# Performance work log

Hardware: AMD Instinct MI355X
Metric: run time of the kernel (lower is better)

Reference implementation:

```python
import jax, jax.numpy as jnp
import numpy as np

N, E, B, D, H, L = 50000, 800000, 16, 64, 128, 2


def _lin(h, w, b):
    return h @ w + b


def _scatter_mean(v, idx, n):
    s = jax.ops.segment_sum(v, idx, num_segments=n)
    c = jax.ops.segment_sum(jnp.ones((v.shape[0],), v.dtype), idx, num_segments=n)
    return s / jnp.maximum(c, 1.0)[:, None]


def setup_inputs() -> dict:
    key = jax.random.key(0)
    ks = iter(jax.random.split(key, 40))

    def p(*shape):
        return jax.random.normal(next(ks), shape, dtype=jnp.float32) * 0.05

    inp = {
        "x": jax.random.normal(next(ks), (N, D), dtype=jnp.float32),
        "edge_attr": jax.random.normal(next(ks), (E, D), dtype=jnp.float32),
        "u": jax.random.normal(next(ks), (B, D), dtype=jnp.float32),
        "e_w1": p(L, 4 * D, H), "e_b1": p(L, H),
        "e_w2": p(L, H, H), "e_b2": p(L, H),
        "e_w3": p(L, H, D), "e_b3": p(L, D),
        "n1_w1": p(L, 2 * D, H), "n1_b1": p(L, H),
        "n1_w2": p(L, H, H), "n1_b2": p(L, H),
        "n2_w1": p(L, D + H + D, H), "n2_b1": p(L, H),
        "n2_w2": p(L, H, D), "n2_b2": p(L, D),
        "g_w1": p(L, 3 * D, H), "g_b1": p(L, H),
        "g_w2": p(L, H, D), "g_b2": p(L, D),
        "edge_index": jax.random.randint(next(ks), (2, E), 0, N, dtype=jnp.int32),
        "batch": jnp.sort(jax.random.randint(next(ks), (N,), 0, B, dtype=jnp.int32)),
    }
    return inp


def _forward(x, edge_attr, u, params, edge_index, batch):
    row, col = edge_index[0], edge_index[1]
    eb = batch[row]  # [E] graph id per edge
    x0, e0, u0 = x, edge_attr, u
    for l in range(L):
        (e_w1, e_b1, e_w2, e_b2, e_w3, e_b3,
         n1_w1, n1_b1, n1_w2, n1_b2,
         n2_w1, n2_b1, n2_w2, n2_b2,
         g_w1, g_b1, g_w2, g_b2) = [pm[l] for pm in params]
        # Edge model: [E, e+2n+u] -> MLP -> [E, D]
        h = jnp.concatenate([x[row], x[col], edge_attr, u[eb]], axis=1)
        h = jax.nn.relu(_lin(h, e_w1, e_b1))
        h = jax.nn.relu(_lin(h, e_w2, e_b2))
        edge_attr = _lin(h, e_w3, e_b3)
        # Node model: gather src node + edge, MLP1, scatter_mean onto dest, MLP2
        se = jnp.concatenate([x[row], edge_attr], axis=1)  # [E, 2D]
        se = _lin(jax.nn.relu(_lin(se, n1_w1, n1_b1)), n1_w2, n1_b2)
        agg = _scatter_mean(se, col, N)  # [N, H]
        xh = jnp.concatenate([x, agg, u[batch]], axis=1)
        x = _lin(jax.nn.relu(_lin(xh, n2_w1, n2_b1)), n2_w2, n2_b2)
        # Global model: per-graph means of updated nodes/edges
        e_agg = _scatter_mean(edge_attr, eb, B)
        n_agg = _scatter_mean(x, batch, B)
        uh = jnp.concatenate([u, n_agg, e_agg], axis=1)
        u = _lin(jax.nn.relu(_lin(uh, g_w1, g_b1)), g_w2, g_b2)
    return x + x0, edge_attr + e0, u + u0


def reference(x, edge_attr, u, e_w1, e_b1, e_w2, e_b2, e_w3, e_b3, n1_w1, n1_b1, n1_w2, n1_b2, n2_w1, n2_b1, n2_w2, n2_b2, g_w1, g_b1, g_w2, g_b2, edge_index, batch):
    params = (e_w1, e_b1, e_w2, e_b2, e_w3, e_b3,
              n1_w1, n1_b1, n1_w2, n1_b2,
              n2_w1, n2_b1, n2_w2, n2_b2,
              g_w1, g_b1, g_w2, g_b2)
    return _forward(x, edge_attr, u, params, edge_index, batch)
```

## Files before the change

kernel.cpp:

```cpp
#include <hip/hip_runtime.h>

#define N_NODES 50000
#define E_EDGES 800000
#define NG 16
#define DD 64
#define HH 128
#define NB_SCAN 49
#define EREP 32

typedef __attribute__((ext_vector_type(8))) __bf16 bf16x8;
typedef __attribute__((ext_vector_type(4))) float f32x4;
typedef unsigned int uint;
typedef unsigned short ushort;
typedef __attribute__((ext_vector_type(4))) uint uint4v;

#define MFMA16(a,b,c) __builtin_amdgcn_mfma_f32_16x16x32_bf16((a),(b),(c),0,0,0)

__device__ __forceinline__ ushort f2bf(float f){
  uint u = __builtin_bit_cast(uint, f);
  u += 0x7fffu + ((u >> 16) & 1u);
  return (ushort)(u >> 16);
}
__device__ __forceinline__ uint pk2(float a, float b){
  return (uint)f2bf(a) | ((uint)f2bf(b) << 16);
}
__device__ __forceinline__ float bflo(uint u){ return __builtin_bit_cast(float, u << 16); }
__device__ __forceinline__ float bfhi(uint u){ return __builtin_bit_cast(float, u & 0xffff0000u); }

__device__ __forceinline__ void bar(){
  asm volatile("s_waitcnt lgkmcnt(0)" ::: "memory");
  __builtin_amdgcn_s_barrier();
}

__device__ __forceinline__ bf16x8 ldfrag(const char* base, int row, int byteoff){
  uint4v v = *(const uint4v*)(base + row*256 + (byteoff ^ ((row & 7) << 4)));
  return __builtin_bit_cast(bf16x8, v);
}
__device__ __forceinline__ uint4v ld_chunk(const char* base, int row, int c16){
  return *(const uint4v*)(base + row*256 + ((c16*16) ^ ((row & 7) << 4)));
}
__device__ __forceinline__ void st_h(char* base, int row, int col, float v){
  *(ushort*)(base + row*256 + ((col*2) ^ ((row & 7) << 4))) = f2bf(v);
}
__device__ __forceinline__ void st_chunk(char* base, int row, int c16, uint4v v){
  *(uint4v*)(base + row*256 + ((c16*16) ^ ((row & 7) << 4))) = v;
}
__device__ __forceinline__ bf16x8 ldfrag128(const char* base, int row, int byteoff){
  uint4v v = *(const uint4v*)(base + row*128 + (byteoff ^ ((row & 7) << 4)));
  return __builtin_bit_cast(bf16x8, v);
}
__device__ __forceinline__ uint4v ld_chunk128(const char* base, int row, int c16){
  return *(const uint4v*)(base + row*128 + ((c16*16) ^ ((row & 7) << 4)));
}
__device__ __forceinline__ void st_chunk128(char* base, int row, int c16, uint4v v){
  *(uint4v*)(base + row*128 + ((c16*16) ^ ((row & 7) << 4))) = v;
}
__device__ __forceinline__ void st_h128(char* base, int row, int col, float v){
  *(ushort*)(base + row*128 + ((col*2) ^ ((row & 7) << 4))) = f2bf(v);
}
__device__ __forceinline__ void pack16_128(char* dst, int r, int c16, const float* src){
  float4 lo = *(const float4*)src;
  float4 hi = *(const float4*)(src + 4);
  uint4v v; v.x = pk2(lo.x, lo.y); v.y = pk2(lo.z, lo.w);
  v.z = pk2(hi.x, hi.y); v.w = pk2(hi.z, hi.w);
  st_chunk128(dst, r, c16, v);
}

__device__ __forceinline__ void stage_b(char* sB, const ushort* wt,
                                        int Nout, int Ktot, int koff, int t, int stride){
  for (int task = t; task < Nout*16; task += stride){
    int n = task >> 4, c = task & 15;
    uint4v v = *(const uint4v*)(wt + (long)n*Ktot + koff + c*8);
    st_chunk(sB, n, c, v);
  }
}
template<int NT>
__device__ __forceinline__ void gemm_acc(const char* A, const char* B,
                                         int wv, int l15, int lhi, f32x4* acc){
  #pragma unroll
  for (int kt = 0; kt < 4; ++kt){
    bf16x8 a = ldfrag(A, wv*16 + l15, kt*64 + lhi*16);
    #pragma unroll
    for (int n = 0; n < NT; ++n){
      bf16x8 bb = ldfrag(B, n*16 + l15, kt*64 + lhi*16);
      acc[n] = MFMA16(a, bb, acc[n]);
    }
  }
}
template<int NT, bool RELU>
__device__ __forceinline__ void epi_lds(char* dst, const f32x4* acc, const float* bias,
                                        int wv, int l15, int lhi){
  #pragma unroll
  for (int n = 0; n < NT; ++n){
    float bv = bias[n*16 + l15];
    #pragma unroll
    for (int j = 0; j < 4; ++j){
      int r = wv*16 + lhi*4 + j;
      float v = acc[n][j] + bv;
      if (RELU) v = fmaxf(v, 0.f);
      st_h(dst, r, n*16 + l15, v);
    }
  }
}

__global__ void convert_x(const float* __restrict__ x, ushort* __restrict__ xbf){
  int i = blockIdx.x*256 + threadIdx.x;
  if (i < (N_NODES*DD)/8){
    float4 lo = *(const float4*)(x + (long)i*8);
    float4 hi = *(const float4*)(x + (long)i*8 + 4);
    uint4v v; v.x = pk2(lo.x, lo.y); v.y = pk2(lo.z, lo.w);
    v.z = pk2(hi.x, hi.y); v.w = pk2(hi.z, hi.w);
    *(uint4v*)(xbf + (long)i*8) = v;
  }
}

__global__ void pack_weights(const float* __restrict__ e1, const float* __restrict__ e2,
                             const float* __restrict__ e3, const float* __restrict__ n12,
                             const float* __restrict__ n21, const float* __restrict__ n22,
                             ushort* __restrict__ out){
  int idx = blockIdx.x * 256 + threadIdx.x;
  int l = idx / 114688, r = idx % 114688;
  const float* src; int K, N, off;
  if      (r <  32768){ src = e1;  K = 256; N = 128; off = 0; }
  else if (r <  49152){ src = e2;  K = 128; N = 128; off = 32768; }
  else if (r <  57344){ src = e3;  K = 128; N = 64;  off = 49152; }
  else if (r <  73728){ src = n12; K = 128; N = 128; off = 57344; }
  else if (r < 106496){ src = n21; K = 256; N = 128; off = 73728; }
  else                { src = n22; K = 128; N = 64;  off = 106496; }
  int q = r - off; int k = q / N; int n = q % N;
  out[(long)l*139264 + off + n*K + k] = f2bf(src[(long)l*K*N + q]);
}

__global__ void make_wc(const float* __restrict__ n1w1, const float* __restrict__ ew3,
                        const float* __restrict__ n1b1, const float* __restrict__ eb3,
                        ushort* __restrict__ packed, float* __restrict__ biasc){
  int l = blockIdx.x, t = threadIdx.x;
  const float* W1 = n1w1 + (long)l*128*128;
  const float* W3 = ew3 + (long)l*128*64;
  ushort* wc = packed + (long)l*139264 + 114688;
  for (int i = t; i < 8192; i += 256){
    int k = i >> 7, n = i & 127;
    wc[n*192 + k] = f2bf(W1[k*128 + n]);
  }
  for (int i = t; i < 16384; i += 256){
    int k2 = i >> 7, n = i & 127;
    float s = 0.f;
    for (int m = 0; m < 64; ++m) s += W3[k2*64 + m] * W1[(64 + m)*128 + n];
    wc[n*192 + 64 + k2] = f2bf(s);
  }
  if (t < 128){
    float s = n1b1[l*128 + t];
    for (int m = 0; m < 64; ++m) s += eb3[l*64 + m] * W1[(64 + m)*128 + t];
    biasc[l*128 + t] = s;
  }
}

__global__ void hist_kernel(const int* __restrict__ edge_index, const int* __restrict__ batch,
                            int* __restrict__ deg, float* __restrict__ cnt_eb){
  __shared__ float h[NG];
  int t = threadIdx.x;
  if (t < NG) h[t] = 0.f;
  __syncthreads();
  int e = blockIdx.x * 256 + t;
  if (e < E_EDGES){
    atomicAdd(deg + edge_index[E_EDGES + e], 1);
    atomicAdd(&h[batch[edge_index[e]]], 1.f);
  }
  __syncthreads();
  if (t < NG) atomicAdd(cnt_eb + t, h[t]);
}
__global__ void count_nodes_kernel(const int* __restrict__ batch, float* __restrict__ cnt_b){
  __shared__ float h[NG];
  int t = threadIdx.x;
  if (t < NG) h[t] = 0.f;
  __syncthreads();
  int n = blockIdx.x * 256 + t;
  if (n < N_NODES) atomicAdd(&h[batch[n]], 1.f);
  __syncthreads();
  if (t < NG) atomicAdd(cnt_b + t, h[t]);
}
__global__ void scan_a(const int* __restrict__ deg, int* __restrict__ bsum){
  __shared__ int red[1024];
  int i = blockIdx.x*1024 + threadIdx.x;
  red[threadIdx.x] = (i < N_NODES) ? deg[i] : 0;
  __syncthreads();
  for (int s = 512; s > 0; s >>= 1){
    if ((int)threadIdx.x < s) red[threadIdx.x] += red[threadIdx.x + s];
    __syncthreads();
  }
  if (threadIdx.x == 0) bsum[blockIdx.x] = red[0];
}
__global__ void scan_b(const int* __restrict__ bsum, int* __restrict__ bbase){
  if (threadIdx.x == 0){
    int run = 0;
    for (int b = 0; b < NB_SCAN; ++b){ int v = bsum[b]; bbase[b] = run; run += v; }
  }
}
__global__ void scan_c(const int* __restrict__ deg, const int* __restrict__ bbase,
                       int* __restrict__ off, int* __restrict__ cursor){
  __shared__ int sc[1024];
  int i = blockIdx.x*1024 + threadIdx.x;
  int v = (i < N_NODES) ? deg[i] : 0;
  sc[threadIdx.x] = v;
  __syncthreads();
  for (int d = 1; d < 1024; d <<= 1){
    int add = ((int)threadIdx.x >= d) ? sc[threadIdx.x - d] : 0;
    __syncthreads();
    sc[threadIdx.x] += add;
    __syncthreads();
  }
  if (i < N_NODES){
    int ex = sc[threadIdx.x] - v + bbase[blockIdx.x];
    off[i] = ex; cursor[i] = ex;
  }
}
__global__ void fill_kernel(const int* __restrict__ edge_index, int* __restrict__ cursor,
                            int* __restrict__ pos){
  int e = blockIdx.x*256 + threadIdx.x;
  if (e < E_EDGES){
    int c = edge_index[E_EDGES + e];
    pos[e] = atomicAdd(&cursor[c], 1);
  }
}

template<bool CSR, bool EBF>
__global__ __launch_bounds__(256, 2) void edge_fused(
    const ushort* __restrict__ xbf, const float* e_f32, const ushort* e_bf,
    const float* __restrict__ u_cur,
    const int* __restrict__ ei, const int* __restrict__ batch,
    const int* __restrict__ pos_arr,
    const ushort* __restrict__ w1t, const ushort* __restrict__ w2t,
    const ushort* __restrict__ w3t, const ushort* __restrict__ wct,
    const ushort* __restrict__ w5t,
    const float* __restrict__ be1, const float* __restrict__ be2,
    const float* __restrict__ be3, const float* __restrict__ biasc,
    const float* __restrict__ bn12,
    float* e_outf, const float* __restrict__ e_resid,
    ushort* __restrict__ se_buf, float* __restrict__ agg_sum,
    float* __restrict__ e_agg_rep, int has_resid)
{
  __shared__ __align__(16) char lds[73728];
  __shared__ float sEagg[NG*DD];
  __shared__ int sRow[64];
  __shared__ int sCol[64];
  __shared__ int sDst[64];
  char* X  = lds;
  char* A0 = lds + 8192;
  char* A1 = lds + 16384;
  char* W0 = lds + 24576;
  char* W1 = lds + 40960;
  char* OV = lds + 57344;
  const int t = threadIdx.x;
  const int wv = t >> 6, l15 = t & 15, lhi = (t >> 4) & 3;
  const int ebase = blockIdx.x * 64;

  auto WSTAGE = [&](char* W, const ushort* wt, int K, int coff){
    #pragma unroll
    for (int it = 0; it < 4; ++it){
      int task = t + it*256, n = task >> 3, c16 = task & 7;
      st_chunk128(W, n, c16, *(const uint4v*)(wt + (long)n*K + coff + c16*8));
    }
  };

  if (t < 64){
    int r = ei[ebase + t];
    int c = ei[E_EDGES + ebase + t];
    sRow[t] = r | (batch[r] << 16);
    sCol[t] = c;
    sDst[t] = CSR ? pos_arr[ebase + t] : c;
  }
  WSTAGE(W0, w1t, 256, 0);
  WSTAGE(W1, w1t, 256, 64);
  bf16x8 b3[4][4];
  #pragma unroll
  for (int n = 0; n < 4; ++n)
    #pragma unroll
    for (int kk = 0; kk < 4; ++kk)
      b3[n][kk] = *(const bf16x8*)(w3t + (long)(n*16 + l15)*128 + kk*32 + lhi*8);
  for (int i = t; i < NG*DD; i += 256) sEagg[i] = 0.f;
  __syncthreads();

  uint4v xr[2], xc[2], eu[2];
  float4 ef[4];
  #pragma unroll
  for (int it = 0; it < 2; ++it){
    int task = t + it*256, r = task >> 3, c16 = task & 7;
    xr[it] = *(const uint4v*)(xbf + (long)(sRow[r] & 0xffff)*DD + c16*8);
    xc[it] = *(const uint4v*)(xbf + (long)sCol[r]*DD + c16*8);
    if (EBF) eu[it] = *(const uint4v*)(e_bf + (long)(ebase + r)*HH + c16*8);
    else { ef[2*it]   = *(const float4*)(e_f32 + (long)(ebase + r)*DD + c16*8);
           ef[2*it+1] = *(const float4*)(e_f32 + (long)(ebase + r)*DD + c16*8 + 4); }
  }
  #pragma unroll
  for (int it = 0; it < 2; ++it){
    int task = t + it*256, r = task >> 3, c16 = task & 7;
    st_chunk128(X, r, c16, xr[it]);
  }
  __syncthreads();

  f32x4 acc1[8];
  #pragma unroll
  for (int n = 0; n < 8; ++n) acc1[n] = f32x4{0,0,0,0};
  auto MM128 = [&](const char* A, const char* W, f32x4* acc){
    #pragma unroll
    for (int kt = 0; kt < 2; ++kt){
      bf16x8 a = ldfrag128(A, wv*16 + l15, kt*64 + lhi*16);
      #pragma unroll
      for (int n = 0; n < 8; ++n){
        bf16x8 bb = ldfrag128(W, n*16 + l15, kt*64 + lhi*16);
        acc[n] = MFMA16(a, bb, acc[n]);
      }
    }
  };
  f32x4 acc3[4];
  #pragma unroll
  for (int n = 0; n < 4; ++n) acc3[n] = f32x4{0,0,0,0};
  auto MMOV = [&](int cbase, const char* W, f32x4* acc){
    #pragma unroll
    for (int kt = 0; kt < 2; ++kt){
      bf16x8 a = ldfrag(OV, wv*16 + l15, cbase + kt*64 + lhi*16);
      #pragma unroll
      for (int n = 0; n < 8; ++n){
        bf16x8 bb = ldfrag128(W, n*16 + l15, kt*64 + lhi*16);
        acc[n] = MFMA16(a, bb, acc[n]);
      }
    }
  };
  auto MMOV3 = [&](int cbase, const char* W, f32x4* acc, int kkb){
    #pragma unroll
    for (int kt = 0; kt < 2; ++kt){
      bf16x8 a = ldfrag(OV, wv*16 + l15, cbase + kt*64 + lhi*16);
      #pragma unroll
      for (int n = 0; n < 8; ++n){
        bf16x8 bb = ldfrag128(W, n*16 + l15, kt*64 + lhi*16);
        acc[n] = MFMA16(a, bb, acc[n]);
      }
      #pragma unroll
      for (int n = 0; n < 4; ++n)
        acc3[n] = MFMA16(a, b3[n][kkb + kt], acc3[n]);
    }
  };
  auto EPI = [&](const float* bias, const f32x4* acc, bool relu){
    #pragma unroll
    for (int n = 0; n < 8; ++n){
      int col = n*16 + l15;
      float bv = bias[col];
      #pragma unroll
      for (int j = 0; j < 4; ++j){
        float v = acc[n][j] + bv;
        if (relu) v = fmaxf(v, 0.f);
        st_h(OV, wv*16 + lhi*4 + j, col, v);
      }
    }
  };

  MM128(X, W0, acc1);
  #pragma unroll
  for (int it = 0; it < 2; ++it){
    int task = t + it*256, r = task >> 3, c16 = task & 7;
    st_chunk128(A0, r, c16, xc[it]);
  }
  bar();
  MM128(A0, W1, acc1);
  WSTAGE(W0, w1t, 256, 128);
  #pragma unroll
  for (int it = 0; it < 2; ++it){
    int task = t + it*256, r = task >> 3, c16 = task & 7;
    if (EBF) st_chunk128(A1, r, c16, eu[it]);
    else {
      uint4v v; v.x = pk2(ef[2*it].x, ef[2*it].y);     v.y = pk2(ef[2*it].z, ef[2*it].w);
      v.z = pk2(ef[2*it+1].x, ef[2*it+1].y); v.w = pk2(ef[2*it+1].z, ef[2*it+1].w);
      st_chunk128(A1, r, c16, v);
    }
  }
  bar();
  MM128(A1, W0, acc1);
  WSTAGE(W1, w1t, 256, 192);
  #pragma unroll
  for (int it = 0; it < 2; ++it){
    int task = t + it*256, r = task >> 3, c16 = task & 7;
    pack16_128(A0, r, c16, u_cur + (long)(sRow[r] >> 16)*DD + c16*8);
  }
  bar();
  MM128(A0, W1, acc1);
  WSTAGE(W0, w2t, 128, 0);
  EPI(be1, acc1, true);
  bar();
  f32x4 acc2[8];
  #pragma unroll
  for (int n = 0; n < 8; ++n) acc2[n] = f32x4{0,0,0,0};
  MMOV(0, W0, acc2);
  WSTAGE(W1, w2t, 128, 64);
  bar();
  MMOV(128, W1, acc2);
  WSTAGE(W0, wct, 192, 0);
  EPI(be2, acc2, true);
  bar();
  f32x4 acc4[8];
  #pragma unroll
  for (int n = 0; n < 8; ++n) acc4[n] = f32x4{0,0,0,0};
  MM128(X, W0, acc4);
  WSTAGE(W1, wct, 192, 64);
  bar();
  MMOV3(0, W1, acc4, 0);
  WSTAGE(W0, wct, 192, 128);
  bar();
  MMOV3(128, W0, acc4, 2);
  WSTAGE(W1, w5t, 128, 0);
  EPI(biasc, acc4, true);
  bar();
  f32x4 acc5[8];
  #pragma unroll
  for (int n = 0; n < 8; ++n) acc5[n] = f32x4{0,0,0,0};
  MMOV(0, W1, acc5);
  WSTAGE(W0, w5t, 128, 64);
  bar();
  MMOV(128, W0, acc5);
  bar();

  if (CSR){
    #pragma unroll
    for (int n = 0; n < 8; ++n){
      int col = n*16 + l15;
      float bv = bn12[col];
      #pragma unroll
      for (int j = 0; j < 4; ++j)
        st_h(OV, wv*16 + lhi*4 + j, col, acc5[n][j] + bv);
    }
    if (!has_resid){
      #pragma unroll
      for (int n = 0; n < 4; ++n){
        int col = n*16 + l15;
        float bv = be3[col];
        #pragma unroll
        for (int j = 0; j < 4; ++j){
          int row = wv*16 + lhi*4 + j;
          float v = acc3[n][j] + bv;
          st_h128(A0, row, col, v);
          atomicAdd(&sEagg[(sRow[row] >> 16)*DD + col], v);
        }
      }
    } else {
      #pragma unroll
      for (int n = 0; n < 4; ++n){
        int col = n*16 + l15;
        float bv = be3[col];
        #pragma unroll
        for (int j = 0; j < 4; ++j){
          int row = wv*16 + lhi*4 + j;
          float v = acc3[n][j] + bv;
          long eg = (long)(ebase + row)*DD + col;
          e_outf[eg] = v + e_resid[eg];
          atomicAdd(&sEagg[(sRow[row] >> 16)*DD + col], v);
        }
      }
    }
    bar();
    #pragma unroll
    for (int it = 0; it < 4; ++it){
      int task = t + it*256, r = task >> 4, c16 = task & 15;
      *(uint4v*)(se_buf + (long)sDst[r]*HH + c16*8) = ld_chunk(OV, r, c16);
    }
    if (!has_resid){
      ushort* ebf_out = (ushort*)e_outf;
      #pragma unroll
      for (int it = 0; it < 2; ++it){
        int task = t + it*256, r = task >> 3, c16 = task & 7;
        *(uint4v*)(ebf_out + (long)(ebase + r)*HH + c16*8) = ld_chunk128(A0, r, c16);
      }
    }
  } else {
    #pragma unroll
    for (int n = 0; n < 8; ++n){
      int col = n*16 + l15;
      float bv = bn12[col];
      #pragma unroll
      for (int j = 0; j < 4; ++j){
        int row = wv*16 + lhi*4 + j;
        atomicAdd(agg_sum + (long)sDst[row]*HH + col, acc5[n][j] + bv);
      }
    }
    #pragma unroll
    for (int n = 0; n < 4; ++n){
      int col = n*16 + l15;
      float bv = be3[col];
      #pragma unroll
      for (int j = 0; j < 4; ++j){
        int row = wv*16 + lhi*4 + j;
        float v = acc3[n][j] + bv;
        long eg = (long)(ebase + row)*DD + col;
        e_outf[eg] = has_resid ? (v + e_resid[eg]) : v;
        atomicAdd(&sEagg[(sRow[row] >> 16)*DD + col], v);
      }
    }
  }
  __syncthreads();
  float* dst = e_agg_rep + (long)(blockIdx.x & (EREP - 1))*NG*DD;
  for (int i = t; i < NG*DD; i += 256) atomicAdd(dst + i, sEagg[i]);
}

template<bool CSR>
__global__ __launch_bounds__(256, 2) void node_kernel(
    const float* __restrict__ x_cur, const float* __restrict__ u_cur,
    const float* __restrict__ x_resid, const int* __restrict__ batch,
    const ushort* __restrict__ se_buf, const int* __restrict__ deg,
    const int* __restrict__ off, const float* __restrict__ agg_sum,
    const ushort* __restrict__ w_n21, const ushort* __restrict__ w_n22,
    const float* __restrict__ b_n21, const float* __restrict__ b_n22,
    float* __restrict__ x_out, ushort* __restrict__ xbf_out,
    float* __restrict__ n_agg, int has_resid)
{
  __shared__ __align__(16) char sA[16384];
  __shared__ __align__(16) char sB[32768];
  __shared__ __align__(16) char sH[16384];
  __shared__ int sBat[64], sDeg[64], sOff[64];
  __shared__ float sRinv[64];
  __shared__ float sNagg[NG*DD];

  const int t = threadIdx.x;
  const int wv = t >> 6, ln = t & 63, l15 = ln & 15, lhi = ln >> 4;
  const int n0 = blockIdx.x * 64;

  if (t < 64){
    int nd = n0 + t;
    int ok = nd < N_NODES;
    sBat[t] = ok ? batch[nd] : 0;
    int d = ok ? deg[nd] : 0;
    sDeg[t] = d;
    sOff[t] = ok ? off[nd] : 0;
    sRinv[t] = 1.f / fmaxf((float)d, 1.f);
  }
  for (int i = t; i < NG*DD; i += 256) sNagg[i] = 0.f;
  __syncthreads();

  float s[32];
  const int r4 = t >> 2, q = t & 3;
  if (CSR){
    #pragma unroll
    for (int k = 0; k < 32; ++k) s[k] = 0.f;
    int d = sDeg[r4], o = sOff[r4];
    for (int i = 0; i < d; ++i){
      const ushort* src = se_buf + (long)(o + i)*HH + q*32;
      #pragma unroll
      for (int c = 0; c < 4; ++c){
        uint4v v = *(const uint4v*)(src + c*8);
        #pragma unroll
        for (int jj = 0; jj < 4; ++jj){
          s[c*8 + jj*2]     += bflo(v[jj]);
          s[c*8 + jj*2 + 1] += bfhi(v[jj]);
        }
      }
    }
    float riv = sRinv[r4];
    #pragma unroll
    for (int k = 0; k < 32; ++k) s[k] *= riv;
  }

  f32x4 acc[8];
  #pragma unroll
  for (int n = 0; n < 8; ++n) acc[n] = f32x4{0.f,0.f,0.f,0.f};

  for (int half = 0; half < 2; ++half){
    if (CSR){
      for (int task = t; task < 512; task += 256){
        int r = task >> 3, c = task & 7;
        int nd = n0 + r;
        bool ok = nd < N_NODES;
        float4 lo = {0,0,0,0}, hi = {0,0,0,0};
        if (ok){
          const float* src = (half == 0) ? (x_cur + (long)nd*DD + c*8)
                                         : (u_cur + (long)sBat[r]*DD + c*8);
          lo = *(const float4*)src; hi = *(const float4*)(src + 4);
        }
        uint4v v; v.x = pk2(lo.x, lo.y); v.y = pk2(lo.z, lo.w);
        v.z = pk2(hi.x, hi.y); v.w = pk2(hi.z, hi.w);
        st_chunk(sA, r, (half == 0) ? c : (8 + c), v);
      }
      if ((half == 0 && q < 2) || (half == 1 && q >= 2)){
        int cbase = (half == 0) ? (8 + q*4) : ((q - 2)*4);
        #pragma unroll
        for (int cc = 0; cc < 4; ++cc){
          uint4v v;
          v.x = pk2(s[cc*8+0], s[cc*8+1]); v.y = pk2(s[cc*8+2], s[cc*8+3]);
          v.z = pk2(s[cc*8+4], s[cc*8+5]); v.w = pk2(s[cc*8+6], s[cc*8+7]);
          st_chunk(sA, r4, cbase + cc, v);
        }
      }
    } else {
      for (int task = t; task < 1024; task += 256){
        int r = task >> 4, c = task & 15;
        int nd = n0 + r;
        bool ok = nd < N_NODES;
        float scale = 1.f;
        const float* src;
        if (half == 0){
          if (c < 8) src = x_cur + (long)nd*DD + c*8;
          else { src = agg_sum + (long)nd*HH + (c-8)*8; scale = sRinv[r]; }
        } else {
          if (c < 8){ src = agg_sum + (long)nd*HH + 64 + c*8; scale = sRinv[r]; }
          else src = u_cur + (long)sBat[r]*DD + (c-8)*8;
        }
        float4 lo = {0,0,0,0}, hi = {0,0,0,0};
        if (ok){ lo = *(const float4*)src; hi = *(const float4*)(src + 4); }
        uint4v v; v.x = pk2(lo.x*scale, lo.y*scale); v.y = pk2(lo.z*scale, lo.w*scale);
        v.z = pk2(hi.x*scale, hi.y*scale); v.w = pk2(hi.z*scale, hi.w*scale);
        st_chunk(sA, r, c, v);
      }
    }
    stage_b(sB, w_n21, 128, 256, half*128, t, 256);
    __syncthreads();
    gemm_acc<8>(sA, sB, wv, l15, lhi, acc);
    __syncthreads();
  }
  epi_lds<8, true>(sH, acc, b_n21, wv, l15, lhi);
  stage_b(sB, w_n22, 64, 128, 0, t, 256);
  __syncthreads();

  f32x4 acc2[4];
  #pragma unroll
  for (int n = 0; n < 4; ++n) acc2[n] = f32x4{0.f,0.f,0.f,0.f};
  gemm_acc<4>(sH, sB, wv, l15, lhi, acc2);

  #pragma unroll
  for (int n = 0; n < 4; ++n){
    float bv = b_n22[n*16 + l15];
    #pragma unroll
    for (int j = 0; j < 4; ++j){
      int r = wv*16 + lhi*4 + j;
      int nd = n0 + r;
      if (nd < N_NODES){
        int col = n*16 + l15;
        float v = acc2[n][j] + bv;
        long xg = (long)nd*DD + col;
        float vw = has_resid ? (v + x_resid[xg]) : v;
        x_out[xg] = vw;
        if (!has_resid) xbf_out[xg] = f2bf(vw);
        atomicAdd(&sNagg[sBat[r]*DD + col], v);
      }
    }
  }
  __syncthreads();
  for (int i = t; i < NG*DD; i += 256) atomicAdd(n_agg + i, sNagg[i]);
}

__global__ void global_kernel(const float* __restrict__ u_cur, const float* __restrict__ n_agg,
                              const float* __restrict__ e_agg_rep, const float* __restrict__ cnt_b,
                              const float* __restrict__ cnt_e,
                              const float* __restrict__ g_w1, const float* __restrict__ g_b1,
                              const float* __restrict__ g_w2, const float* __restrict__ g_b2,
                              const float* __restrict__ u_resid, float* __restrict__ u_out,
                              int has_resid)
{
  int g = blockIdx.x, t = threadIdx.x;
  __shared__ float uh[192];
  __shared__ float hb[128];
  float v;
  if (t < 64)       v = u_cur[g*64 + t];
  else if (t < 128) v = n_agg[g*64 + (t-64)] / fmaxf(cnt_b[g], 1.f);
  else {
    float s = 0.f;
    for (int c = 0; c < EREP; ++c) s += e_agg_rep[c*NG*DD + g*64 + (t-128)];
    v = s / fmaxf(cnt_e[g], 1.f);
  }
  uh[t] = v;
  __syncthreads();
  if (t < 128){
    float s = g_b1[t];
    for (int k = 0; k < 192; ++k) s += uh[k] * g_w1[k*128 + t];
    hb[t] = fmaxf(s, 0.f);
  }
  __syncthreads();
  if (t < 64){
    float s = g_b2[t];
    for (int k = 0; k < 128; ++k) s += hb[k] * g_w2[k*64 + t];
    if (has_resid) s += u_resid[g*64 + t];
    u_out[g*64 + t] = s;
  }
}

extern "C" void kernel_launch(void* const* d_in, const int* in_sizes, int n_in,
                              void* d_out, int out_size, void* d_ws, size_t ws_size,
                              hipStream_t stream)
{
  const float* x0   = (const float*)d_in[0];
  const float* e0   = (const float*)d_in[1];
  const float* u0   = (const float*)d_in[2];
  const float* e_w1 = (const float*)d_in[3];
  const float* e_b1 = (const float*)d_in[4];
  const float* e_w2 = (const float*)d_in[5];
  const float* e_b2 = (const float*)d_in[6];
  const float* e_w3 = (const float*)d_in[7];
  const float* e_b3 = (const float*)d_in[8];
  const float* n1_w1 = (const float*)d_in[9];
  const float* n1_b1 = (const float*)d_in[10];
  const float* n1_w2 = (const float*)d_in[11];
  const float* n1_b2 = (const float*)d_in[12];
  const float* n2_w1 = (const float*)d_in[13];
  const float* n2_b1 = (const float*)d_in[14];
  const float* n2_w2 = (const float*)d_in[15];
  const float* n2_b2 = (const float*)d_in[16];
  const float* g_w1 = (const float*)d_in[17];
  const float* g_b1 = (const float*)d_in[18];
  const float* g_w2 = (const float*)d_in[19];
  const float* g_b2 = (const float*)d_in[20];
  const int* edge_index = (const int*)d_in[21];
  const int* batch      = (const int*)d_in[22];

  float* out_x = (float*)d_out;
  float* out_e = out_x + (long)N_NODES*DD;
  float* out_u = out_e + (long)E_EDGES*DD;

  char* ws = (char*)d_ws;
  int*   deg    = (int*)(ws + 0);
  int*   off    = (int*)(ws + 200000);
  int*   cursor = (int*)(ws + 400000);
  int*   bsum   = (int*)(ws + 600000);
  int*   bbase  = (int*)(ws + 600256);
  float* cnt_eb = (float*)(ws + 600512);
  float* cnt_b  = (float*)(ws + 600576);
  float* n_agg  = (float*)(ws + 604736);
  float* biascf = (float*)(ws + 608832);
  ushort* packed = (ushort*)(ws + 609856);
  float* e_agg_rep = (float*)(ws + 1166912);
  ushort* xbf = (ushort*)(ws + 1297984);
  const size_t big = 7697984;
  bool use_csr = ws_size >= (size_t)(big + 204800000 + 3200000);
  ushort* se_buf = (ushort*)(ws + big);
  int*    pos    = (int*)(ws + big + 204800000);
  float*  agg_sum = (float*)(ws + big);

  (void)hipMemsetAsync(deg, 0, 200000, stream);
  (void)hipMemsetAsync(cnt_eb, 0, 128, stream);
  pack_weights<<<896, 256, 0, stream>>>(e_w1, e_w2, e_w3, n1_w2, n2_w1, n2_w2, packed);
  make_wc<<<2, 256, 0, stream>>>(n1_w1, e_w3, n1_b1, e_b3, packed, biascf);
  hist_kernel<<<3125, 256, 0, stream>>>(edge_index, batch, deg, cnt_eb);
  count_nodes_kernel<<<196, 256, 0, stream>>>(batch, cnt_b);
  convert_x<<<1563, 256, 0, stream>>>(x0, xbf);
  if (use_csr){
    scan_a<<<NB_SCAN, 1024, 0, stream>>>(deg, bsum);
    scan_b<<<1, 64, 0, stream>>>(bsum, bbase);
    scan_c<<<NB_SCAN, 1024, 0, stream>>>(deg, bbase, off, cursor);
    fill_kernel<<<3125, 256, 0, stream>>>(edge_index, cursor, pos);
  }

  const float* xc = x0;
  const float* uc = u0;
  for (int l = 0; l < 2; ++l){
    (void)hipMemsetAsync(n_agg, 0, 4096, stream);
    (void)hipMemsetAsync(e_agg_rep, 0, EREP*NG*DD*4, stream);
    if (!use_csr){
      (void)hipMemsetAsync(agg_sum, 0, (size_t)N_NODES*HH*4, stream);
      if (l == 1) convert_x<<<1563, 256, 0, stream>>>(xc, xbf);
    }
    const ushort* P = packed + (long)l*139264;
    const float* ef32 = (l == 0) ? e0 : out_e;
    if (use_csr){
      if (l == 0)
        edge_fused<true, false><<<12500, 256, 0, stream>>>(
            xbf, e0, (const ushort*)out_e, uc, edge_index, batch, pos,
            P + 0, P + 32768, P + 49152, P + 114688, P + 57344,
            e_b1, e_b2, e_b3, biascf, n1_b2,
            out_e, e0, se_buf, agg_sum, e_agg_rep, 0);
      else
        edge_fused<true, true><<<12500, 256, 0, stream>>>(
            xbf, ef32, (const ushort*)out_e, uc, edge_index, batch, pos,
            P + 0, P + 32768, P + 49152, P + 114688, P + 57344,
            e_b1 + 128, e_b2 + 128, e_b3 + 64, biascf + 128, n1_b2 + 128,
            out_e, e0, se_buf, agg_sum, e_agg_rep, 1);
      node_kernel<true><<<782, 256, 0, stream>>>(
          xc, uc, x0, batch, se_buf, deg, off, agg_sum,
          P + 73728, P + 106496, n2_b1 + l*128, n2_b2 + l*64,
          out_x, xbf, n_agg, l == 1);
    } else {
      edge_fused<false, false><<<12500, 256, 0, stream>>>(
          xbf, ef32, (const ushort*)out_e, uc, edge_index, batch, pos,
          P + 0, P + 32768, P + 49152, P + 114688, P + 57344,
          e_b1 + l*128, e_b2 + l*128, e_b3 + l*64, biascf + l*128, n1_b2 + l*128,
          out_e, e0, se_buf, agg_sum, e_agg_rep, l == 1);
      node_kernel<false><<<782, 256, 0, stream>>>(
          xc, uc, x0, batch, se_buf, deg, off, agg_sum,
          P + 73728, P + 106496, n2_b1 + l*128, n2_b2 + l*64,
          out_x, xbf, n_agg, l == 1);
    }
    global_kernel<<<NG, 192, 0, stream>>>(
        uc, n_agg, e_agg_rep, cnt_b, cnt_eb,
        g_w1 + l*192*128, g_b1 + l*128, g_w2 + l*128*64, g_b2 + l*64,
        u0, out_u, l == 1);
    xc = out_x; uc = out_u;
  }
}
```

Before: 1.767 ms.

## Stage edge-kernel weights via async global_load_lds with double-buffered prefetch

Replaces the register round-trip weight staging (global load into VGPRs, then LDS store) with direct global-to-LDS 16-byte loads, issued one stage ahead so each weight tile streams in while the previous MFMA stage runs. vmcnt waits plus barriers replace the implicit dependency, and the XOR swizzle is applied on the global source address instead. The u_cur gather is also hoisted into the initial load batch so its latency overlaps earlier work. In exchange it relies on precise vmcnt counting and barrier placement; a miscount would race on the W0/W1 buffers.

```diff
diff --git a/kernel.cpp b/kernel.cpp
--- a/kernel.cpp
+++ b/kernel.cpp
@@ -30,6 +30,13 @@
 __device__ __forceinline__ void bar(){
   asm volatile("s_waitcnt lgkmcnt(0)" ::: "memory");
   __builtin_amdgcn_s_barrier();
+}
+#define VMWAIT(n) asm volatile("s_waitcnt vmcnt(" #n ")" ::: "memory")
+
+__device__ __forceinline__ void gload16(const void* g, void* l){
+  __builtin_amdgcn_global_load_lds(
+      (const __attribute__((address_space(1))) unsigned int*)g,
+      (__attribute__((address_space(3))) unsigned int*)l, 16, 0, 0);
 }
 
 __device__ __forceinline__ bf16x8 ldfrag(const char* base, int row, int byteoff){
@@ -251,14 +258,16 @@
   char* W1 = lds + 40960;
   char* OV = lds + 57344;
   const int t = threadIdx.x;
-  const int wv = t >> 6, l15 = t & 15, lhi = (t >> 4) & 3;
+  const int wv = t >> 6, lane = t & 63, l15 = t & 15, lhi = (t >> 4) & 3;
   const int ebase = blockIdx.x * 64;
 
-  auto WSTAGE = [&](char* W, const ushort* wt, int K, int coff){
+  auto GL = [&](const ushort* base, long stride, int koff, char* slot){
     #pragma unroll
     for (int it = 0; it < 4; ++it){
-      int task = t + it*256, n = task >> 3, c16 = task & 7;
-      st_chunk128(W, n, c16, *(const uint4v*)(wt + (long)n*K + coff + c16*8));
+      int q = (wv*4 + it)*64 + lane;
+      int r = q >> 3, cp = q & 7;
+      gload16(base + (long)r*stride + koff + ((cp ^ (r & 7))*8),
+              slot + (wv*4 + it)*1024);
     }
   };
 
@@ -269,8 +278,8 @@
     sCol[t] = c;
     sDst[t] = CSR ? pos_arr[ebase + t] : c;
   }
-  WSTAGE(W0, w1t, 256, 0);
-  WSTAGE(W1, w1t, 256, 64);
+  GL(w1t, 256, 0, W0);
+  GL(w1t, 256, 64, W1);
   bf16x8 b3[4][4];
   #pragma unroll
   for (int n = 0; n < 4; ++n)
@@ -281,7 +290,7 @@
   __syncthreads();
 
   uint4v xr[2], xc[2], eu[2];
-  float4 ef[4];
+  float4 ef[4], uu[4];
   #pragma unroll
   for (int it = 0; it < 2; ++it){
     int task = t + it*256, r = task >> 3, c16 = task & 7;
@@ -290,6 +299,8 @@
     if (EBF) eu[it] = *(const uint4v*)(e_bf + (long)(ebase + r)*HH + c16*8);
     else { ef[2*it]   = *(const float4*)(e_f32 + (long)(ebase + r)*DD + c16*8);
            ef[2*it+1] = *(const float4*)(e_f32 + (long)(ebase + r)*DD + c16*8 + 4); }
+    uu[2*it]   = *(const float4*)(u_cur + (long)(sRow[r] >> 16)*DD + c16*8);
+    uu[2*it+1] = *(const float4*)(u_cur + (long)(sRow[r] >> 16)*DD + c16*8 + 4);
   }
   #pragma unroll
   for (int it = 0; it < 2; ++it){
@@ -361,8 +372,8 @@
     st_chunk128(A0, r, c16, xc[it]);
   }
   bar();
+  GL(w1t, 256, 128, W0);
   MM128(A0, W1, acc1);
-  WSTAGE(W0, w1t, 256, 128);
   #pragma unroll
   for (int it = 0; it < 2; ++it){
     int task = t + it*256, r = task >> 3, c16 = task & 7;
@@ -374,47 +385,58 @@
     }
   }
   bar();
+  GL(w1t, 256, 192, W1);
+  VMWAIT(4); __builtin_amdgcn_s_barrier();
   MM128(A1, W0, acc1);
-  WSTAGE(W1, w1t, 256, 192);
   #pragma unroll
   for (int it = 0; it < 2; ++it){
     int task = t + it*256, r = task >> 3, c16 = task & 7;
-    pack16_128(A0, r, c16, u_cur + (long)(sRow[r] >> 16)*DD + c16*8);
-  }
-  bar();
+    uint4v v; v.x = pk2(uu[2*it].x, uu[2*it].y);     v.y = pk2(uu[2*it].z, uu[2*it].w);
+    v.z = pk2(uu[2*it+1].x, uu[2*it+1].y); v.w = pk2(uu[2*it+1].z, uu[2*it+1].w);
+    st_chunk128(A0, r, c16, v);
+  }
+  bar();
+  GL(w2t, 128, 0, W0);
+  VMWAIT(4); __builtin_amdgcn_s_barrier();
   MM128(A0, W1, acc1);
-  WSTAGE(W0, w2t, 128, 0);
   EPI(be1, acc1, true);
   bar();
+  GL(w2t, 128, 64, W1);
+  VMWAIT(4); __builtin_amdgcn_s_barrier();
   f32x4 acc2[8];
   #pragma unroll
   for (int n = 0; n < 8; ++n) acc2[n] = f32x4{0,0,0,0};
   MMOV(0, W0, acc2);
-  WSTAGE(W1, w2t, 128, 64);
-  bar();
+  bar();
+  GL(wct, 192, 0, W0);
+  VMWAIT(4); __builtin_amdgcn_s_barrier();
   MMOV(128, W1, acc2);
-  WSTAGE(W0, wct, 192, 0);
   EPI(be2, acc2, true);
   bar();
+  GL(wct, 192, 64, W1);
+  VMWAIT(4); __builtin_amdgcn_s_barrier();
   f32x4 acc4[8];
   #pragma unroll
   for (int n = 0; n < 8; ++n) acc4[n] = f32x4{0,0,0,0};
   MM128(X, W0, acc4);
-  WSTAGE(W1, wct, 192, 64);
-  bar();
+  bar();
+  GL(wct, 192, 128, W0);
+  VMWAIT(4); __builtin_amdgcn_s_barrier();
   MMOV3(0, W1, acc4, 0);
-  WSTAGE(W0, wct, 192, 128);
-  bar();
+  bar();
+  GL(w5t, 128, 0, W1);
+  VMWAIT(4); __builtin_amdgcn_s_barrier();
   MMOV3(128, W0, acc4, 2);
-  WSTAGE(W1, w5t, 128, 0);
   EPI(biasc, acc4, true);
   bar();
+  GL(w5t, 128, 64, W0);
+  VMWAIT(4); __builtin_amdgcn_s_barrier();
   f32x4 acc5[8];
   #pragma unroll
   for (int n = 0; n < 8; ++n) acc5[n] = f32x4{0,0,0,0};
   MMOV(0, W1, acc5);
-  WSTAGE(W0, w5t, 128, 64);
-  bar();
+  bar();
+  VMWAIT(0); __builtin_amdgcn_s_barrier();
   MMOV(128, W0, acc5);
   bar();
 
```

Result: no change. 1.797 ms (+1.6%).
